# Optimization experiments

Hardware: AMD Instinct MI355X
Metric: run time of the kernel (lower is better)

The kernel has to match this reference:

```python
import jax, jax.numpy as jnp
import numpy as np

N_NODES = 100000
N_EDGES = 1600000
IN_CH = 128
HID = 128
N_GRAPHS = 256


def gcn_conv(x, W, b, src, dst, n_nodes):
    """PyG GCNConv: linear -> symmetric degree normalization with self-loops -> scatter-add -> bias."""
    h = x @ W  # [N, H]
    # degree (in-degree on target index) including the added self-loop
    deg = 1.0 + jax.ops.segment_sum(jnp.ones((dst.shape[0],), x.dtype), dst, num_segments=n_nodes)
    dis = deg ** -0.5  # deg >= 1, no inf guard needed
    coef = dis[src] * dis[dst]  # [E]
    agg = jax.ops.segment_sum(h[src] * coef[:, None], dst, num_segments=n_nodes)
    # self-loop contribution: h[i] * dis[i]^2 = h[i] / deg[i]
    agg = agg + h * (1.0 / deg)[:, None]
    return agg + b


def global_mean_pool(x, batch, n_graphs):
    sums = jax.ops.segment_sum(x, batch, num_segments=n_graphs)
    cnts = jax.ops.segment_sum(jnp.ones((x.shape[0],), x.dtype), batch, num_segments=n_graphs)
    return sums / jnp.maximum(cnts, 1.0)[:, None]


def setup_inputs() -> dict:
    key = jax.random.key(0)
    ks = jax.random.split(key, 8)
    x = jax.random.normal(ks[0], (N_NODES, IN_CH), dtype=jnp.float32)
    edge_index = jax.random.randint(ks[1], (2, N_EDGES), 0, N_NODES, dtype=jnp.int32)
    batch = jnp.sort(jax.random.randint(ks[2], (N_NODES,), 0, N_GRAPHS, dtype=jnp.int32))
    # glorot-ish init for weights
    s1 = (6.0 / (IN_CH + HID)) ** 0.5
    W1 = jax.random.uniform(ks[3], (IN_CH, HID), jnp.float32, -s1, s1)
    b1 = jnp.zeros((HID,), jnp.float32)
    s2 = (6.0 / (HID + HID)) ** 0.5
    W2 = jax.random.uniform(ks[4], (HID, HID), jnp.float32, -s2, s2)
    b2 = jnp.zeros((HID,), jnp.float32)
    s3 = (6.0 / (HID + 1)) ** 0.5
    Wfc = jax.random.uniform(ks[5], (HID, 1), jnp.float32, -s3, s3)
    bfc = jnp.zeros((1,), jnp.float32)
    return {"x": x, "edge_index": edge_index, "batch": batch,
            "W1": W1, "b1": b1, "W2": W2, "b2": b2, "Wfc": Wfc, "bfc": bfc}


def reference(x, edge_index, batch, W1, b1, W2, b2, Wfc, bfc):
    src, dst = edge_index[0], edge_index[1]
    h = jax.nn.relu(gcn_conv(x, W1, b1, src, dst, N_NODES))
    h = jax.nn.relu(gcn_conv(h, W2, b2, src, dst, N_NODES))
    g = global_mean_pool(h, batch, N_GRAPHS)  # [G, H]
    out = g @ Wfc + bfc  # [G, 1]
    return out.squeeze(-1)
```

## Files before the change

kernel.cpp:

```cpp
#include <hip/hip_runtime.h>

#define N_NODES 100000
#define N_EDGES 1600000
#define HID 128
#define N_GRAPHS 256
#define POOL_BLOCKS 512

#define BSHIFT 9
#define BSIZE 512
#define NBUCK ((N_NODES + BSIZE - 1) / BSIZE)
#define BCAP 10240
#define EPB 8192
#define NBLK_A ((N_EDGES + EPB - 1) / EPB)

typedef unsigned int uint;
typedef unsigned short ushort;
typedef short short8 __attribute__((ext_vector_type(8)));
typedef float f32x4 __attribute__((ext_vector_type(4)));

__device__ __forceinline__ float bf2f(ushort u) {
    return __uint_as_float(((uint)u) << 16);
}
__device__ __forceinline__ ushort f2bf(float f) {
    uint u = __float_as_uint(f);
    u += 0x7FFFu + ((u >> 16) & 1u);
    return (ushort)(u >> 16);
}
__device__ __forceinline__ uint4 pack8(const float* r) {
    uint4 o;
    o.x = (uint)f2bf(r[0]) | ((uint)f2bf(r[1]) << 16);
    o.y = (uint)f2bf(r[2]) | ((uint)f2bf(r[3]) << 16);
    o.z = (uint)f2bf(r[4]) | ((uint)f2bf(r[5]) << 16);
    o.w = (uint)f2bf(r[6]) | ((uint)f2bf(r[7]) << 16);
    return o;
}
__device__ __forceinline__ void accp(uint4 v, float2* a) {
    a[0].x += __uint_as_float(v.x << 16);
    a[0].y += __uint_as_float(v.x & 0xFFFF0000u);
    a[1].x += __uint_as_float(v.y << 16);
    a[1].y += __uint_as_float(v.y & 0xFFFF0000u);
    a[2].x += __uint_as_float(v.z << 16);
    a[2].y += __uint_as_float(v.z & 0xFFFF0000u);
    a[3].x += __uint_as_float(v.w << 16);
    a[3].y += __uint_as_float(v.w & 0xFFFF0000u);
}

union Frag16 {
    uint4 u;
    short8 s;
    ushort h[8];
};

__global__ void zero_kernel(int* __restrict__ p, int n) {
    int i = blockIdx.x * blockDim.x + threadIdx.x;
    if (i < n) p[i] = 0;
}

__global__ __launch_bounds__(256) void bucket_scatter_kernel(const int* __restrict__ src,
                                                             const int* __restrict__ dst,
                                                             int* __restrict__ bfill,
                                                             uint* __restrict__ bucketed) {
    __shared__ int h[NBUCK];
    __shared__ int rb[NBUCK];
    for (int t = threadIdx.x; t < NBUCK; t += 256) h[t] = 0;
    __syncthreads();
    int base = blockIdx.x * EPB;
#pragma unroll 4
    for (int it = 0; it < EPB / 256; ++it) {
        int e = base + it * 256 + threadIdx.x;
        if (e < N_EDGES) atomicAdd(&h[dst[e] >> BSHIFT], 1);
    }
    __syncthreads();
    for (int t = threadIdx.x; t < NBUCK; t += 256) {
        rb[t] = (h[t] ? atomicAdd(&bfill[t], h[t]) : 0) + t * BCAP;
        h[t] = 0;
    }
    __syncthreads();
#pragma unroll 4
    for (int it = 0; it < EPB / 256; ++it) {
        int e = base + it * 256 + threadIdx.x;
        if (e < N_EDGES) {
            int d = dst[e];
            int b = d >> BSHIFT;
            int pos = rb[b] + atomicAdd(&h[b], 1);
            bucketed[pos] = (uint)src[e] | ((uint)(d & (BSIZE - 1)) << 17);
        }
    }
}

__global__ __launch_bounds__(256) void bucket_csr_kernel(const uint* __restrict__ bucketed,
                                                         const int* __restrict__ bfill,
                                                         int* __restrict__ degi,
                                                         int* __restrict__ rowptr,
                                                         float* __restrict__ dis,
                                                         uint* __restrict__ csrb) {
    int b = blockIdx.x;
    int beg = b * BCAP;
    int ne = bfill[b];
    __shared__ int cnt[BSIZE];
    __shared__ int fl[BSIZE];
    __shared__ int ex[BSIZE];
    __shared__ int ps[256];
    int t = threadIdx.x;
    cnt[t] = 0; cnt[t + 256] = 0;
    fl[t] = 0;  fl[t + 256] = 0;
    __syncthreads();
    for (int i = t; i < ne; i += 256) atomicAdd(&cnt[bucketed[beg + i] >> 17], 1);
    __syncthreads();
    int v0 = cnt[2 * t], v1 = cnt[2 * t + 1];
    int s = v0 + v1;
    ps[t] = s;
    __syncthreads();
    for (int off = 1; off < 256; off <<= 1) {
        int a = (t >= off) ? ps[t - off] : 0;
        __syncthreads();
        ps[t] += a;
        __syncthreads();
    }
    int e0 = ps[t] - s;
    ex[2 * t] = e0;
    ex[2 * t + 1] = e0 + v0;
    int g = b * BSIZE + 2 * t;
    if (g < N_NODES) {
        degi[g] = v0; rowptr[g] = beg + e0;
        dis[g] = rsqrtf(1.0f + (float)v0);
    }
    if (g + 1 < N_NODES) {
        degi[g + 1] = v1; rowptr[g + 1] = beg + e0 + v0;
        dis[g + 1] = rsqrtf(1.0f + (float)v1);
    }
    __syncthreads();
    for (int i = t; i < ne; i += 256) {
        uint u = bucketed[beg + i];
        int dl = u >> 17;
        int p = ex[dl] + atomicAdd(&fl[dl], 1);
        csrb[beg + p] = (u & 0x1FFFFu) << 8;
    }
}

__global__ void prep_wfrag2(const float* __restrict__ W1, const float* __restrict__ W2,
                            uint4* __restrict__ WB1, uint4* __restrict__ WB2) {
    int t = blockIdx.x * 256 + threadIdx.x;
    if (t >= 4096) return;
    const float* W = (t < 2048) ? W1 : W2;
    uint4* WB = (t < 2048) ? WB1 : WB2;
    int tt = t & 2047;
    int lane = tt & 63;
    int nt = (tt >> 6) & 7;
    int kt = tt >> 9;
    int kbase = kt * 32 + (lane >> 4) * 8;
    int col = nt * 16 + (lane & 15);
    float r[8];
#pragma unroll
    for (int j = 0; j < 8; j++) r[j] = W[(size_t)(kbase + j) * 128 + col];
    WB[tt] = pack8(r);
}

template <bool F32IN>
__global__ __launch_bounds__(256) void mgemm_kernel(const void* __restrict__ Xv,
                                                    const uint4* __restrict__ WB,
                                                    const float* __restrict__ dis,
                                                    ushort* __restrict__ Y, int M) {
    __shared__ uint4 WBs[2048];
#pragma unroll
    for (int i = 0; i < 8; i++) WBs[i * 256 + threadIdx.x] = WB[i * 256 + threadIdx.x];
    __syncthreads();

    int wave = threadIdx.x >> 6;
    int lane = threadIdx.x & 63;
    int r0 = blockIdx.x * 128 + wave * 32;
    if (r0 >= M) return;

    int rowA = lane & 15;
    int ksub = (lane >> 4) * 8;

    Frag16 a[2][4];
#pragma unroll
    for (int rt = 0; rt < 2; ++rt) {
        int row = r0 + rt * 16 + rowA;
        if (F32IN) {
            const float* xr = (const float*)Xv + (size_t)row * 128;
#pragma unroll
            for (int kt = 0; kt < 4; ++kt) {
                float4 lo = *(const float4*)(xr + kt * 32 + ksub);
                float4 hi = *(const float4*)(xr + kt * 32 + ksub + 4);
                float r[8] = {lo.x, lo.y, lo.z, lo.w, hi.x, hi.y, hi.z, hi.w};
                a[rt][kt].u = pack8(r);
            }
        } else {
            const uint4* xr = (const uint4*)Xv + (size_t)row * 16;
#pragma unroll
            for (int kt = 0; kt < 4; ++kt) a[rt][kt].u = xr[kt * 4 + (lane >> 4)];
        }
    }

    f32x4 acc[2][8];
#pragma unroll
    for (int rt = 0; rt < 2; ++rt)
#pragma unroll
        for (int nt = 0; nt < 8; ++nt) acc[rt][nt] = (f32x4){0.f, 0.f, 0.f, 0.f};

#pragma unroll
    for (int kt = 0; kt < 4; ++kt) {
#pragma unroll
        for (int nt = 0; nt < 8; ++nt) {
            Frag16 b;
            b.u = WBs[(kt * 8 + nt) * 64 + lane];
            acc[0][nt] = __builtin_amdgcn_mfma_f32_16x16x32_bf16(a[0][kt].s, b.s, acc[0][nt], 0, 0, 0);
            acc[1][nt] = __builtin_amdgcn_mfma_f32_16x16x32_bf16(a[1][kt].s, b.s, acc[1][nt], 0, 0, 0);
        }
    }

    int cbase = lane & 15;
#pragma unroll
    for (int rt = 0; rt < 2; ++rt) {
        int rbase = r0 + rt * 16 + (lane >> 4) * 4;
        float d0 = dis[rbase + 0], d1 = dis[rbase + 1];
        float d2 = dis[rbase + 2], d3 = dis[rbase + 3];
#pragma unroll
        for (int nt = 0; nt < 8; ++nt) {
            Y[(size_t)(rbase + 0) * 128 + nt * 16 + cbase] = f2bf(acc[rt][nt][0] * d0);
            Y[(size_t)(rbase + 1) * 128 + nt * 16 + cbase] = f2bf(acc[rt][nt][1] * d1);
            Y[(size_t)(rbase + 2) * 128 + nt * 16 + cbase] = f2bf(acc[rt][nt][2] * d2);
            Y[(size_t)(rbase + 3) * 128 + nt * 16 + cbase] = f2bf(acc[rt][nt][3] * d3);
        }
    }
}

__global__ __launch_bounds__(256) void aggregate_kernel(
    const ushort* __restrict__ T, const uint* __restrict__ csrb,
    const int* __restrict__ rowptr, const int* __restrict__ degi,
    const float* __restrict__ dis, const float* __restrict__ bias,
    ushort* __restrict__ H) {
    int node = blockIdx.x * 4 + (threadIdx.x >> 6);
    int lane = threadIdx.x & 63;
    if (node >= N_NODES) return;
    int group = lane >> 4;
    uint sub16 = (uint)(lane & 15) * 16u;

    int start = rowptr[node];
    int cnt = degi[node];
    const char* Tb = (const char*)T;

    float2 acc[4];
#pragma unroll
    for (int i = 0; i < 4; i++) acc[i] = make_float2(0.f, 0.f);

    int j = group;
    for (; j + 12 < cnt; j += 16) {
        uint o0 = csrb[start + j];
        uint o1 = csrb[start + j + 4];
        uint o2 = csrb[start + j + 8];
        uint o3 = csrb[start + j + 12];
        uint4 v0 = *(const uint4*)(Tb + (o0 + sub16));
        uint4 v1 = *(const uint4*)(Tb + (o1 + sub16));
        uint4 v2 = *(const uint4*)(Tb + (o2 + sub16));
        uint4 v3 = *(const uint4*)(Tb + (o3 + sub16));
        accp(v0, acc); accp(v1, acc); accp(v2, acc); accp(v3, acc);
    }
    for (; j < cnt; j += 4) {
        uint o0 = csrb[start + j];
        uint4 v0 = *(const uint4*)(Tb + (o0 + sub16));
        accp(v0, acc);
    }

#pragma unroll
    for (int i = 0; i < 4; i++) {
        acc[i].x += __shfl_xor(acc[i].x, 16);
        acc[i].y += __shfl_xor(acc[i].y, 16);
        acc[i].x += __shfl_xor(acc[i].x, 32);
        acc[i].y += __shfl_xor(acc[i].y, 32);
    }

    if (group == 0) {
        uint4 sv = *(const uint4*)(Tb + (((uint)node << 8) + sub16));
        accp(sv, acc);
        float di = dis[node];
        int sub = lane & 15;
        float4 blo = ((const float4*)bias)[sub * 2];
        float4 bhi = ((const float4*)bias)[sub * 2 + 1];
        float bb[8] = {blo.x, blo.y, blo.z, blo.w, bhi.x, bhi.y, bhi.z, bhi.w};
        float r[8];
        float af[8] = {acc[0].x, acc[0].y, acc[1].x, acc[1].y,
                       acc[2].x, acc[2].y, acc[3].x, acc[3].y};
#pragma unroll
        for (int i = 0; i < 8; i++) r[i] = fmaxf(di * af[i] + bb[i], 0.f);
        ((uint4*)H)[(size_t)node * 16 + sub] = pack8(r);
    }
}

__global__ __launch_bounds__(256) void pool_kernel(const ushort* __restrict__ H,
                                                   const int* __restrict__ batch,
                                                   const float* __restrict__ Wfc,
                                                   float* __restrict__ gsum) {
    int wave = threadIdx.x >> 6;
    int lane = threadIdx.x & 63;
    int wid = blockIdx.x * 4 + wave;
    const int nwaves = POOL_BLOCKS * 4;
    const int per = (N_NODES + nwaves - 1) / nwaves;
    int start = wid * per;
    int end = min(start + per, N_NODES);
    if (start >= end) return;

    const uint* H1 = (const uint*)H;
    float2 w = ((const float2*)Wfc)[lane];
    float2 acc = make_float2(0.f, 0.f);
    int gcur = batch[start];

    for (int node = start; node < end; ++node) {
        int g = batch[node];
        if (g != gcur) {
            float d = acc.x * w.x + acc.y * w.y;
#pragma unroll
            for (int off = 32; off > 0; off >>= 1) d += __shfl_down(d, off);
            if (lane == 0) atomicAdd(&gsum[gcur], d);
            acc = make_float2(0.f, 0.f);
            gcur = g;
        }
        uint v = H1[(size_t)node * 64 + lane];
        acc.x += bf2f((ushort)(v & 0xFFFF));
        acc.y += bf2f((ushort)(v >> 16));
    }
    float d = acc.x * w.x + acc.y * w.y;
#pragma unroll
    for (int off = 32; off > 0; off >>= 1) d += __shfl_down(d, off);
    if (lane == 0) atomicAdd(&gsum[gcur], d);
}

__global__ void finalize_kernel(const float* __restrict__ gsum, const int* __restrict__ batch,
                                const float* __restrict__ bfc, float* __restrict__ out) {
    int g = threadIdx.x;
    if (g >= N_GRAPHS) return;
    auto lb = [&](int key) {
        int lo = 0, hi = N_NODES;
        while (lo < hi) {
            int mid = (lo + hi) >> 1;
            if (batch[mid] < key) lo = mid + 1; else hi = mid;
        }
        return lo;
    };
    int a = lb(g), b = lb(g + 1);
    float cnt = (float)(b - a);
    out[g] = gsum[g] / fmaxf(cnt, 1.0f) + bfc[0];
}

extern "C" void kernel_launch(void* const* d_in, const int* in_sizes, int n_in,
                              void* d_out, int out_size, void* d_ws, size_t ws_size,
                              hipStream_t stream) {
    const float* x    = (const float*)d_in[0];
    const int*   eidx = (const int*)d_in[1];
    const int*   batch= (const int*)d_in[2];
    const float* W1   = (const float*)d_in[3];
    const float* b1   = (const float*)d_in[4];
    const float* W2   = (const float*)d_in[5];
    const float* b2   = (const float*)d_in[6];
    const float* Wfc  = (const float*)d_in[7];
    const float* bfc  = (const float*)d_in[8];
    float* out = (float*)d_out;

    const int* src = eidx;
    const int* dst = eidx + N_EDGES;

    size_t off = 0;
    char* base = (char*)d_ws;
    auto alloc = [&](size_t bytes) -> void* {
        void* p = base + off;
        off += (bytes + 255) & ~(size_t)255;
        return p;
    };
    int*    bfill  = (int*)alloc(NBUCK * 4);
    float*  gsum   = (float*)alloc(N_GRAPHS * 4);
    size_t zero_bytes = off;
    ushort* A      = (ushort*)alloc((size_t)N_NODES * HID * 2);
    ushort* B      = (ushort*)alloc((size_t)N_NODES * HID * 2);
    int*    degi   = (int*)alloc(N_NODES * 4);
    int*    rowptr = (int*)alloc(N_NODES * 4);
    float*  dis    = (float*)alloc(N_NODES * 4);
    uint*   csrb   = (uint*)alloc((size_t)NBUCK * BCAP * 4);
    uint*   bucketed = (uint*)alloc((size_t)NBUCK * BCAP * 4);
    uint4*  WB1    = (uint4*)alloc(2048 * 16);
    uint4*  WB2    = (uint4*)alloc(2048 * 16);

    int zn = (int)(zero_bytes / 4);
    zero_kernel<<<(zn + 255) / 256, 256, 0, stream>>>((int*)base, zn);

    bucket_scatter_kernel<<<NBLK_A, 256, 0, stream>>>(src, dst, bfill, bucketed);
    bucket_csr_kernel<<<NBUCK, 256, 0, stream>>>(bucketed, bfill, degi, rowptr, dis, csrb);

    prep_wfrag2<<<16, 256, 0, stream>>>(W1, W2, WB1, WB2);

    int gemm_grid = (N_NODES + 127) / 128;
    int agg_grid  = (N_NODES + 3) / 4;

    mgemm_kernel<true><<<gemm_grid, 256, 0, stream>>>(x, WB1, dis, A, N_NODES);
    aggregate_kernel<<<agg_grid, 256, 0, stream>>>(A, csrb, rowptr, degi, dis, b1, B);
    mgemm_kernel<false><<<gemm_grid, 256, 0, stream>>>(B, WB2, dis, A, N_NODES);
    aggregate_kernel<<<agg_grid, 256, 0, stream>>>(A, csrb, rowptr, degi, dis, b2, B);

    pool_kernel<<<POOL_BLOCKS, 256, 0, stream>>>(B, batch, Wfc, gsum);
    finalize_kernel<<<1, 256, 0, stream>>>(gsum, batch, bfc, out);
}
```

Baseline: 254.0 us.

## Fuse mean-pool projection into second aggregation and coalesce GEMM stores via LDS

The second aggregation kernel now projects each node's output onto Wfc and atomically adds per-graph partial sums directly, removing the separate pool kernel and the write and re-read of the final hidden features. The GEMM epilogue stages bf16 results in shared memory and writes full 16-byte row chunks instead of scattered 2-byte stores. bf16 conversion now uses the HIP intrinsic. This adds one atomic per block and relies on N_NODES being divisible by 4, since the bounds check was removed.

```diff
diff --git a/kernel.cpp b/kernel.cpp
--- a/kernel.cpp
+++ b/kernel.cpp
@@ -1,10 +1,10 @@
 #include <hip/hip_runtime.h>
+#include <hip/hip_bf16.h>
 
 #define N_NODES 100000
 #define N_EDGES 1600000
 #define HID 128
 #define N_GRAPHS 256
-#define POOL_BLOCKS 512
 
 #define BSHIFT 9
 #define BSIZE 512
@@ -18,20 +18,17 @@
 typedef short short8 __attribute__((ext_vector_type(8)));
 typedef float f32x4 __attribute__((ext_vector_type(4)));
 
-__device__ __forceinline__ float bf2f(ushort u) {
-    return __uint_as_float(((uint)u) << 16);
-}
-__device__ __forceinline__ ushort f2bf(float f) {
-    uint u = __float_as_uint(f);
-    u += 0x7FFFu + ((u >> 16) & 1u);
-    return (ushort)(u >> 16);
+__device__ __forceinline__ ushort f2bf_hw(float f) {
+    union { __hip_bfloat16 b; ushort u; } cv;
+    cv.b = __float2bfloat16(f);
+    return cv.u;
 }
 __device__ __forceinline__ uint4 pack8(const float* r) {
     uint4 o;
-    o.x = (uint)f2bf(r[0]) | ((uint)f2bf(r[1]) << 16);
-    o.y = (uint)f2bf(r[2]) | ((uint)f2bf(r[3]) << 16);
-    o.z = (uint)f2bf(r[4]) | ((uint)f2bf(r[5]) << 16);
-    o.w = (uint)f2bf(r[6]) | ((uint)f2bf(r[7]) << 16);
+    o.x = (uint)f2bf_hw(r[0]) | ((uint)f2bf_hw(r[1]) << 16);
+    o.y = (uint)f2bf_hw(r[2]) | ((uint)f2bf_hw(r[3]) << 16);
+    o.z = (uint)f2bf_hw(r[4]) | ((uint)f2bf_hw(r[5]) << 16);
+    o.w = (uint)f2bf_hw(r[6]) | ((uint)f2bf_hw(r[7]) << 16);
     return o;
 }
 __device__ __forceinline__ void accp(uint4 v, float2* a) {
@@ -162,6 +159,7 @@
                                                     const float* __restrict__ dis,
                                                     ushort* __restrict__ Y, int M) {
     __shared__ uint4 WBs[2048];
+    __shared__ ushort stage[4][16][136];
 #pragma unroll
     for (int i = 0; i < 8; i++) WBs[i * 256 + threadIdx.x] = WB[i * 256 + threadIdx.x];
     __syncthreads();
@@ -212,29 +210,45 @@
     }
 
     int cbase = lane & 15;
+    int rbl = (lane >> 4) * 4;
+    ushort* sp = &stage[wave][0][0];
+    char* Yb = (char*)Y;
 #pragma unroll
     for (int rt = 0; rt < 2; ++rt) {
-        int rbase = r0 + rt * 16 + (lane >> 4) * 4;
+        int r0g = r0 + rt * 16;
+        int rbase = r0g + rbl;
         float d0 = dis[rbase + 0], d1 = dis[rbase + 1];
         float d2 = dis[rbase + 2], d3 = dis[rbase + 3];
 #pragma unroll
         for (int nt = 0; nt < 8; ++nt) {
-            Y[(size_t)(rbase + 0) * 128 + nt * 16 + cbase] = f2bf(acc[rt][nt][0] * d0);
-            Y[(size_t)(rbase + 1) * 128 + nt * 16 + cbase] = f2bf(acc[rt][nt][1] * d1);
-            Y[(size_t)(rbase + 2) * 128 + nt * 16 + cbase] = f2bf(acc[rt][nt][2] * d2);
-            Y[(size_t)(rbase + 3) * 128 + nt * 16 + cbase] = f2bf(acc[rt][nt][3] * d3);
-        }
-    }
-}
-
+            int col = nt * 16 + cbase;
+            sp[(rbl + 0) * 136 + col] = f2bf_hw(acc[rt][nt][0] * d0);
+            sp[(rbl + 1) * 136 + col] = f2bf_hw(acc[rt][nt][1] * d1);
+            sp[(rbl + 2) * 136 + col] = f2bf_hw(acc[rt][nt][2] * d2);
+            sp[(rbl + 3) * 136 + col] = f2bf_hw(acc[rt][nt][3] * d3);
+        }
+#pragma unroll
+        for (int i = 0; i < 4; ++i) {
+            int idx = i * 64 + lane;
+            int row = idx >> 4, c16 = idx & 15;
+            uint4 v = *(const uint4*)(sp + row * 136 + c16 * 8);
+            *(uint4*)(Yb + (size_t)(r0g + row) * 256 + c16 * 16) = v;
+        }
+    }
+}
+
+template <int POOL>
 __global__ __launch_bounds__(256) void aggregate_kernel(
     const ushort* __restrict__ T, const uint* __restrict__ csrb,
     const int* __restrict__ rowptr, const int* __restrict__ degi,
     const float* __restrict__ dis, const float* __restrict__ bias,
-    ushort* __restrict__ H) {
-    int node = blockIdx.x * 4 + (threadIdx.x >> 6);
+    ushort* __restrict__ H, const int* __restrict__ batch,
+    const float* __restrict__ Wfc, float* __restrict__ gsum) {
+    __shared__ float pd[4];
+    __shared__ int   pg[4];
+    int wave = threadIdx.x >> 6;
+    int node = blockIdx.x * 4 + wave;
     int lane = threadIdx.x & 63;
-    if (node >= N_NODES) return;
     int group = lane >> 4;
     uint sub16 = (uint)(lane & 15) * 16u;
 
@@ -285,46 +299,32 @@
                        acc[2].x, acc[2].y, acc[3].x, acc[3].y};
 #pragma unroll
         for (int i = 0; i < 8; i++) r[i] = fmaxf(di * af[i] + bb[i], 0.f);
-        ((uint4*)H)[(size_t)node * 16 + sub] = pack8(r);
-    }
-}
-
-__global__ __launch_bounds__(256) void pool_kernel(const ushort* __restrict__ H,
-                                                   const int* __restrict__ batch,
-                                                   const float* __restrict__ Wfc,
-                                                   float* __restrict__ gsum) {
-    int wave = threadIdx.x >> 6;
-    int lane = threadIdx.x & 63;
-    int wid = blockIdx.x * 4 + wave;
-    const int nwaves = POOL_BLOCKS * 4;
-    const int per = (N_NODES + nwaves - 1) / nwaves;
-    int start = wid * per;
-    int end = min(start + per, N_NODES);
-    if (start >= end) return;
-
-    const uint* H1 = (const uint*)H;
-    float2 w = ((const float2*)Wfc)[lane];
-    float2 acc = make_float2(0.f, 0.f);
-    int gcur = batch[start];
-
-    for (int node = start; node < end; ++node) {
-        int g = batch[node];
-        if (g != gcur) {
-            float d = acc.x * w.x + acc.y * w.y;
-#pragma unroll
-            for (int off = 32; off > 0; off >>= 1) d += __shfl_down(d, off);
-            if (lane == 0) atomicAdd(&gsum[gcur], d);
-            acc = make_float2(0.f, 0.f);
-            gcur = g;
-        }
-        uint v = H1[(size_t)node * 64 + lane];
-        acc.x += bf2f((ushort)(v & 0xFFFF));
-        acc.y += bf2f((ushort)(v >> 16));
-    }
-    float d = acc.x * w.x + acc.y * w.y;
-#pragma unroll
-    for (int off = 32; off > 0; off >>= 1) d += __shfl_down(d, off);
-    if (lane == 0) atomicAdd(&gsum[gcur], d);
+        if (POOL == 0) {
+            ((uint4*)H)[(size_t)node * 16 + sub] = pack8(r);
+        } else {
+            float4 wlo = ((const float4*)Wfc)[sub * 2];
+            float4 whi = ((const float4*)Wfc)[sub * 2 + 1];
+            float d = r[0] * wlo.x + r[1] * wlo.y + r[2] * wlo.z + r[3] * wlo.w
+                    + r[4] * whi.x + r[5] * whi.y + r[6] * whi.z + r[7] * whi.w;
+            d += __shfl_xor(d, 1);
+            d += __shfl_xor(d, 2);
+            d += __shfl_xor(d, 4);
+            d += __shfl_xor(d, 8);
+            if (sub == 0) { pd[wave] = d; pg[wave] = batch[node]; }
+        }
+    }
+    if (POOL == 1) {
+        __syncthreads();
+        if (threadIdx.x == 0) {
+            float s = pd[0]; int g = pg[0];
+#pragma unroll
+            for (int w = 1; w < 4; ++w) {
+                if (pg[w] == g) s += pd[w];
+                else { atomicAdd(&gsum[g], s); g = pg[w]; s = pd[w]; }
+            }
+            atomicAdd(&gsum[g], s);
+        }
+    }
 }
 
 __global__ void finalize_kernel(const float* __restrict__ gsum, const int* __restrict__ batch,
@@ -390,13 +390,14 @@
     prep_wfrag2<<<16, 256, 0, stream>>>(W1, W2, WB1, WB2);
 
     int gemm_grid = (N_NODES + 127) / 128;
-    int agg_grid  = (N_NODES + 3) / 4;
+    int agg_grid  = N_NODES / 4;
 
     mgemm_kernel<true><<<gemm_grid, 256, 0, stream>>>(x, WB1, dis, A, N_NODES);
-    aggregate_kernel<<<agg_grid, 256, 0, stream>>>(A, csrb, rowptr, degi, dis, b1, B);
+    aggregate_kernel<0><<<agg_grid, 256, 0, stream>>>(A, csrb, rowptr, degi, dis, b1, B,
+                                                      batch, Wfc, gsum);
     mgemm_kernel<false><<<gemm_grid, 256, 0, stream>>>(B, WB2, dis, A, N_NODES);
-    aggregate_kernel<<<agg_grid, 256, 0, stream>>>(A, csrb, rowptr, degi, dis, b2, B);
-
-    pool_kernel<<<POOL_BLOCKS, 256, 0, stream>>>(B, batch, Wfc, gsum);
+    aggregate_kernel<1><<<agg_grid, 256, 0, stream>>>(A, csrb, rowptr, degi, dis, b2, B,
+                                                      batch, Wfc, gsum);
+
     finalize_kernel<<<1, 256, 0, stream>>>(gsum, batch, bfc, out);
 }
```

New measurement: 298.1 us. 17.4% more time.
